# Performance work log

Hardware: AMD Instinct MI355X
Metric: run time of the kernel (lower is better)

Reference implementation:

```python
import jax, jax.numpy as jnp
import numpy as np

N = 100000          # n_nodes
E = 3200000         # n_edges (avg degree 32)
IN_FEATS = 256
H = 128             # h_feats
N_HOPS = 4


def setup_inputs() -> dict:
    key = jax.random.key(0)
    ks = jax.random.split(key, 8)
    edge_index = jax.random.randint(ks[0], (2, E), 0, N, dtype=jnp.int32)
    features = jax.random.normal(ks[1], (N, IN_FEATS), dtype=jnp.float32)
    # input block: Linear(in_feats, h_feats)
    W0 = jax.random.normal(ks[2], (IN_FEATS, H), dtype=jnp.float32) / np.sqrt(IN_FEATS)
    b0 = jnp.zeros((H,), jnp.float32)
    # per-hop GCNConv bias (weight=False because RN=='attentive')
    biases = jnp.zeros((N_HOPS, H), jnp.float32)
    # per-hop attention gate: Linear(2*h_feats, 1) + tanh
    Watt = jax.random.normal(ks[3], (N_HOPS, 2 * H), dtype=jnp.float32) / np.sqrt(2 * H)
    batt = jnp.zeros((N_HOPS,), jnp.float32)
    return {"edge_index": edge_index, "features": features,
            "W0": W0, "b0": b0, "biases": biases, "Watt": Watt, "batt": batt}


def _gcn_agg(x, src, dst):
    # symmetric GCN normalization with self-loops: D^-1/2 (A+I) D^-1/2 @ x
    deg = jnp.zeros((N,), x.dtype).at[dst].add(1.0) + 1.0  # +1 for self-loop
    dinv = jax.lax.rsqrt(deg)
    w = dinv[src] * dinv[dst]                               # [E]
    out = jnp.zeros((N, x.shape[1]), x.dtype).at[dst].add(x[src] * w[:, None])
    return out + x * (dinv * dinv)[:, None]                 # self-loop term


def reference(edge_index, features, W0, b0, biases, Watt, batt):
    src, dst = edge_index[0], edge_index[1]
    # hop-0 input block (dropout=0, norm=Identity)
    h = jax.nn.relu(features @ W0 + b0)                     # [N, H]
    for i in range(N_HOPS):
        # GCNConv with weight=False: aggregation + bias + act
        h_k = jax.nn.relu(_gcn_agg(h, src, dst) + biases[i])
        # attentive hop combination: a = tanh(Linear([h_k, h]))
        a = jnp.tanh(jnp.concatenate([h_k, h], axis=-1) @ Watt[i] + batt[i])[:, None]
        h = a * h_k + (1.0 - a) * h
    return h
```

## Files before the change

### kernel.cpp

```cpp
#include <hip/hip_runtime.h>
#include <hip/hip_fp16.h>
#include <math.h>

#define N_NODES 100000
#define N_EDGES 3200000
#define IN_F 256
#define H 128
#define N_HOPS 4
#define SCAN_B 256
#define GB_M 128
#define GB_K 32


__global__ void deg_kernel(const int* __restrict__ dst, int* __restrict__ deg) {
    int e = blockIdx.x * blockDim.x + threadIdx.x;
    if (e < N_EDGES) atomicAdd(&deg[dst[e]], 1);
}

__global__ void dinv_kernel(const int* __restrict__ deg, float* __restrict__ dinv) {
    int n = blockIdx.x * blockDim.x + threadIdx.x;
    if (n < N_NODES) dinv[n] = rsqrtf((float)deg[n] + 1.0f);
}

__global__ void scan_p1(const int* __restrict__ deg, int* __restrict__ bsum) {
    __shared__ int s[SCAN_B];
    int n = blockIdx.x * SCAN_B + threadIdx.x;
    s[threadIdx.x] = (n < N_NODES) ? deg[n] : 0;
    __syncthreads();
    for (int off = SCAN_B / 2; off; off >>= 1) {
        if (threadIdx.x < off) s[threadIdx.x] += s[threadIdx.x + off];
        __syncthreads();
    }
    if (threadIdx.x == 0) bsum[blockIdx.x] = s[0];
}

__global__ void scan_p2(int* __restrict__ bsum, int nb) {
    __shared__ int s[512];
    int t = threadIdx.x;
    int v0 = (t < nb) ? bsum[t] : 0;
    s[t] = v0;
    __syncthreads();
    for (int off = 1; off < 512; off <<= 1) {
        int v = (t >= off) ? s[t - off] : 0;
        __syncthreads();
        s[t] += v;
        __syncthreads();
    }
    if (t < nb) bsum[t] = s[t] - v0;
}

__global__ void scan_p3(const int* __restrict__ deg, const int* __restrict__ boff,
                        int* __restrict__ rowptr) {
    __shared__ int s[SCAN_B];
    int n = blockIdx.x * SCAN_B + threadIdx.x;
    int v = (n < N_NODES) ? deg[n] : 0;
    s[threadIdx.x] = v;
    __syncthreads();
    for (int off = 1; off < SCAN_B; off <<= 1) {
        int t = (threadIdx.x >= off) ? s[threadIdx.x - off] : 0;
        __syncthreads();
        s[threadIdx.x] += t;
        __syncthreads();
    }
    int incl = s[threadIdx.x];
    int excl = incl - v;
    if (n < N_NODES) rowptr[n] = boff[blockIdx.x] + excl;
    if (n == N_NODES - 1) rowptr[N_NODES] = boff[blockIdx.x] + incl;
}

__global__ void scatter_kernel(const int* __restrict__ src, const int* __restrict__ dst,
                               const float* __restrict__ dinv, const int* __restrict__ rowptr,
                               int* __restrict__ cursor, uint2* __restrict__ edges) {
    int e = blockIdx.x * blockDim.x + threadIdx.x;
    if (e >= N_EDGES) return;
    int s = src[e], d = dst[e];
    int pos = rowptr[d] + atomicAdd(&cursor[d], 1);
    edges[pos] = make_uint2((unsigned)s, __float_as_uint(dinv[s] * dinv[d]));
}

__global__ __launch_bounds__(256) void input_gemm(const float* __restrict__ X,
                                                  const float* __restrict__ W0,
                                                  const float* __restrict__ b0,
                                                  __half* __restrict__ h16) {
    __shared__ float AsT[GB_K][GB_M + 4];
    __shared__ float Ws[GB_K][H];
    int node0 = blockIdx.x * GB_M;
    int tid = threadIdx.x;
    int tx = tid & 15;
    int ty = tid >> 4;

    float acc[8][8];
#pragma unroll
    for (int i = 0; i < 8; ++i)
#pragma unroll
        for (int j = 0; j < 8; ++j) acc[i][j] = 0.f;

    for (int k0 = 0; k0 < IN_F; k0 += GB_K) {
#pragma unroll
        for (int j = 0; j < 4; ++j) {
            int idx = tid + 256 * j;
            int row = idx >> 3, c4 = idx & 7;
            float4 v = make_float4(0.f, 0.f, 0.f, 0.f);
            if (node0 + row < N_NODES)
                v = *(const float4*)(X + (size_t)(node0 + row) * IN_F + k0 + c4 * 4);
            AsT[c4 * 4 + 0][row] = v.x;
            AsT[c4 * 4 + 1][row] = v.y;
            AsT[c4 * 4 + 2][row] = v.z;
            AsT[c4 * 4 + 3][row] = v.w;
        }
#pragma unroll
        for (int j = 0; j < 4; ++j) {
            int idx = tid + 256 * j;
            int row = idx >> 5, c4 = idx & 31;
            *(float4*)&Ws[row][c4 * 4] = *(const float4*)(W0 + (size_t)(k0 + row) * H + c4 * 4);
        }
        __syncthreads();
#pragma unroll
        for (int kk = 0; kk < GB_K; ++kk) {
            float a[8], w[8];
            *(float4*)&a[0] = *(const float4*)&AsT[kk][ty * 8];
            *(float4*)&a[4] = *(const float4*)&AsT[kk][ty * 8 + 4];
            *(float4*)&w[0] = *(const float4*)&Ws[kk][tx * 8];
            *(float4*)&w[4] = *(const float4*)&Ws[kk][tx * 8 + 4];
#pragma unroll
            for (int i = 0; i < 8; ++i)
#pragma unroll
                for (int j = 0; j < 8; ++j) acc[i][j] += a[i] * w[j];
        }
        __syncthreads();
    }

#pragma unroll
    for (int i = 0; i < 8; ++i) {
        int n = node0 + ty * 8 + i;
        if (n < N_NODES) {
            union { float4 f4; __half2 h2[4]; } u;
#pragma unroll
            for (int jj = 0; jj < 4; ++jj) {
                float v0 = acc[i][2 * jj + 0] + b0[tx * 8 + 2 * jj + 0];
                float v1 = acc[i][2 * jj + 1] + b0[tx * 8 + 2 * jj + 1];
                v0 = v0 > 0.f ? v0 : 0.f;
                v1 = v1 > 0.f ? v1 : 0.f;
                u.h2[jj] = __floats2half2_rn(v0, v1);
            }
            *(float4*)(h16 + (size_t)n * H + tx * 8) = u.f4;
        }
    }
}

__global__ __launch_bounds__(256) void hop_kernel(const __half* __restrict__ h_in,
                                                  __half* __restrict__ h16_out,
                                                  float* __restrict__ out32,
                                                  const int* __restrict__ rowptr,
                                                  const uint2* __restrict__ edges,
                                                  const float* __restrict__ dinv,
                                                  const float* __restrict__ bias,
                                                  const float* __restrict__ Wa,
                                                  const float* __restrict__ batt) {
    int wid = threadIdx.x >> 6;
    int lane = threadIdx.x & 63;
    int n = blockIdx.x * 4 + wid;
    if (n >= N_NODES) return;

    float2 hn = __half22float2(((const __half2*)(h_in + (size_t)n * H))[lane]);
    float dd = dinv[n];
    dd = dd * dd;
    float accx = hn.x * dd, accy = hn.y * dd;

    int e0 = rowptr[n], e1 = rowptr[n + 1];
    for (int base = e0; base < e1; base += 64) {
        int cnt = e1 - base;
        if (cnt > 64) cnt = 64;
        int sv = 0;
        float wv = 0.f;
        if (lane < cnt) {
            uint2 ev = edges[base + lane];
            sv = (int)ev.x;
            wv = __uint_as_float(ev.y);
        }
        int j = 0;
        for (; j + 3 < cnt; j += 4) {
            int s0 = __shfl(sv, j + 0), s1 = __shfl(sv, j + 1);
            int s2 = __shfl(sv, j + 2), s3 = __shfl(sv, j + 3);
            float w0 = __shfl(wv, j + 0), w1 = __shfl(wv, j + 1);
            float w2 = __shfl(wv, j + 2), w3 = __shfl(wv, j + 3);
            float2 g0 = __half22float2(((const __half2*)(h_in + (size_t)s0 * H))[lane]);
            float2 g1 = __half22float2(((const __half2*)(h_in + (size_t)s1 * H))[lane]);
            float2 g2 = __half22float2(((const __half2*)(h_in + (size_t)s2 * H))[lane]);
            float2 g3 = __half22float2(((const __half2*)(h_in + (size_t)s3 * H))[lane]);
            accx += w0 * g0.x + w1 * g1.x + w2 * g2.x + w3 * g3.x;
            accy += w0 * g0.y + w1 * g1.y + w2 * g2.y + w3 * g3.y;
        }
        for (; j < cnt; ++j) {
            int sj = __shfl(sv, j);
            float wj = __shfl(wv, j);
            float2 g = __half22float2(((const __half2*)(h_in + (size_t)sj * H))[lane]);
            accx += wj * g.x;
            accy += wj * g.y;
        }
    }

    float hkx = accx + bias[2 * lane];     hkx = hkx > 0.f ? hkx : 0.f;
    float hky = accy + bias[2 * lane + 1]; hky = hky > 0.f ? hky : 0.f;

    float p = hkx * Wa[2 * lane] + hky * Wa[2 * lane + 1]
            + hn.x * Wa[H + 2 * lane] + hn.y * Wa[H + 2 * lane + 1];
#pragma unroll
    for (int off = 32; off; off >>= 1) p += __shfl_xor(p, off);
    float a = tanhf(p + batt[0]);

    float ox = a * hkx + (1.f - a) * hn.x;
    float oy = a * hky + (1.f - a) * hn.y;
    if (out32) {
        ((float2*)(out32 + (size_t)n * H))[lane] = make_float2(ox, oy);
    } else {
        ((__half2*)(h16_out + (size_t)n * H))[lane] = __floats2half2_rn(ox, oy);
    }
}


extern "C" void kernel_launch(void* const* d_in, const int* in_sizes, int n_in,
                              void* d_out, int out_size, void* d_ws, size_t ws_size,
                              hipStream_t stream) {
    const int* edge_index = (const int*)d_in[0];
    const int* src = edge_index;
    const int* dst = edge_index + N_EDGES;
    const float* features = (const float*)d_in[1];
    const float* W0 = (const float*)d_in[2];
    const float* b0 = (const float*)d_in[3];
    const float* biases = (const float*)d_in[4];
    const float* Watt = (const float*)d_in[5];
    const float* batt = (const float*)d_in[6];
    float* out = (float*)d_out;

    size_t off = 0;
    char* base = (char*)d_ws;
    auto carve = [&](size_t bytes) -> void* {
        void* q = base + off;
        off += (bytes + 255) & ~(size_t)255;
        return q;
    };
    int* deg = (int*)carve((size_t)N_NODES * 4);
    float* dinv = (float*)carve((size_t)N_NODES * 4);
    int* rowptr = (int*)carve((size_t)(N_NODES + 1) * 4);
    int* cursor = (int*)carve((size_t)N_NODES * 4);
    int* bsum = (int*)carve(4096);
    uint2* edges = (uint2*)carve((size_t)N_EDGES * 8);
    __half* h16A = (__half*)carve((size_t)N_NODES * H * 2);
    __half* h16B = (__half*)carve((size_t)N_NODES * H * 2);

    hipMemsetAsync(deg, 0, (size_t)N_NODES * 4, stream);
    hipMemsetAsync(cursor, 0, (size_t)N_NODES * 4, stream);

    int eb = (N_EDGES + 255) / 256;
    int nbN = (N_NODES + 255) / 256;
    deg_kernel<<<eb, 256, 0, stream>>>(dst, deg);
    dinv_kernel<<<nbN, 256, 0, stream>>>(deg, dinv);
    scan_p1<<<nbN, SCAN_B, 0, stream>>>(deg, bsum);
    scan_p2<<<1, 512, 0, stream>>>(bsum, nbN);
    scan_p3<<<nbN, SCAN_B, 0, stream>>>(deg, bsum, rowptr);
    scatter_kernel<<<eb, 256, 0, stream>>>(src, dst, dinv, rowptr, cursor, edges);

    input_gemm<<<(N_NODES + GB_M - 1) / GB_M, 256, 0, stream>>>(features, W0, b0, h16A);

    __half* hin = h16A;
    __half* hout = h16B;
    for (int i = 0; i < N_HOPS; ++i) {
        bool last = (i == N_HOPS - 1);
        hop_kernel<<<(N_NODES + 3) / 4, 256, 0, stream>>>(
            hin, hout, last ? out : nullptr, rowptr, edges, dinv,
            biases + (size_t)i * H, Watt + (size_t)i * 2 * H, batt + i);
        __half* t = hin; hin = hout; hout = t;
    }
}
```

Measured before the change: 999.0 us.

## Use two-pass bucketed CSR scatter and MFMA fp16 input GEMM

The single random-scatter CSR build is replaced by two passes. Edges are first binned into buckets of 32 destination nodes, then scattered within each bucket, which improves locality of the atomics and writes. The FP32 SIMT input GEMM is replaced by an MFMA 16x16x32 fp16 GEMM with swizzled LDS tiles, and W0 is converted and transposed to fp16 in a prep kernel. This adds an extra pass over the edges and an fp16 rounding of the inputs. The temporary edge buffer reuses the h16B allocation.

```diff
diff --git a/kernel.cpp b/kernel.cpp
--- a/kernel.cpp
+++ b/kernel.cpp
@@ -8,8 +8,11 @@
 #define H 128
 #define N_HOPS 4
 #define SCAN_B 256
-#define GB_M 128
-#define GB_K 32
+#define BSH 5
+#define NBUCK ((N_NODES + 31) >> BSH)
+
+typedef _Float16 half8_t __attribute__((ext_vector_type(8)));
+typedef float f32x4 __attribute__((ext_vector_type(4)));
 
 
 __global__ void deg_kernel(const int* __restrict__ dst, int* __restrict__ deg) {
@@ -68,84 +71,123 @@
     if (n == N_NODES - 1) rowptr[N_NODES] = boff[blockIdx.x] + incl;
 }
 
-__global__ void scatter_kernel(const int* __restrict__ src, const int* __restrict__ dst,
-                               const float* __restrict__ dinv, const int* __restrict__ rowptr,
-                               int* __restrict__ cursor, uint2* __restrict__ edges) {
+__global__ void bucket_p1(const int* __restrict__ src, const int* __restrict__ dst,
+                          const int* __restrict__ rowptr, int* __restrict__ bcur,
+                          uint2* __restrict__ tmp) {
     int e = blockIdx.x * blockDim.x + threadIdx.x;
     if (e >= N_EDGES) return;
     int s = src[e], d = dst[e];
+    int b = d >> BSH;
+    int pos = rowptr[b << BSH] + atomicAdd(&bcur[b], 1);
+    tmp[pos] = make_uint2((unsigned)s, (unsigned)d);
+}
+
+__global__ void scatter2(const uint2* __restrict__ tmp, const float* __restrict__ dinv,
+                         const int* __restrict__ rowptr, int* __restrict__ cursor,
+                         uint2* __restrict__ edges) {
+    int e = blockIdx.x * blockDim.x + threadIdx.x;
+    if (e >= N_EDGES) return;
+    uint2 ev = tmp[e];
+    int s = (int)ev.x, d = (int)ev.y;
     int pos = rowptr[d] + atomicAdd(&cursor[d], 1);
-    edges[pos] = make_uint2((unsigned)s, __float_as_uint(dinv[s] * dinv[d]));
-}
-
-__global__ __launch_bounds__(256) void input_gemm(const float* __restrict__ X,
-                                                  const float* __restrict__ W0,
-                                                  const float* __restrict__ b0,
-                                                  __half* __restrict__ h16) {
-    __shared__ float AsT[GB_K][GB_M + 4];
-    __shared__ float Ws[GB_K][H];
-    int node0 = blockIdx.x * GB_M;
+    edges[pos] = make_uint2(ev.x, __float_as_uint(dinv[s] * dinv[d]));
+}
+
+__global__ void w16_kernel(const float* __restrict__ W0, _Float16* __restrict__ W16t) {
+    int t = blockIdx.x * 256 + threadIdx.x;
+    if (t < H * IN_F) {
+        int n = t >> 8;
+        int k = t & 255;
+        W16t[(size_t)n * IN_F + k] = (_Float16)W0[(size_t)k * H + n];
+    }
+}
+
+__global__ __launch_bounds__(256) void mfma_gemm(const float* __restrict__ X,
+                                                 const _Float16* __restrict__ W16t,
+                                                 const float* __restrict__ b0,
+                                                 __half* __restrict__ h16) {
+    __shared__ _Float16 Al[128 * 64];
+    __shared__ _Float16 Bl[128 * 64];
     int tid = threadIdx.x;
-    int tx = tid & 15;
-    int ty = tid >> 4;
-
-    float acc[8][8];
-#pragma unroll
-    for (int i = 0; i < 8; ++i)
-#pragma unroll
-        for (int j = 0; j < 8; ++j) acc[i][j] = 0.f;
-
-    for (int k0 = 0; k0 < IN_F; k0 += GB_K) {
+    int wv = tid >> 6, ln = tid & 63;
+    size_t node0 = (size_t)blockIdx.x * 128;
+
+    f32x4 acc[2][8];
+#pragma unroll
+    for (int mi = 0; mi < 2; ++mi)
+#pragma unroll
+        for (int ni = 0; ni < 8; ++ni) acc[mi][ni] = (f32x4)(0.f);
+
+    int arow = tid >> 1;
+    int koff = (tid & 1) * 32;
+    bool arow_ok = (node0 + (size_t)arow) < N_NODES;
+
+    for (int k0 = 0; k0 < IN_F; k0 += 64) {
 #pragma unroll
         for (int j = 0; j < 4; ++j) {
-            int idx = tid + 256 * j;
-            int row = idx >> 3, c4 = idx & 7;
-            float4 v = make_float4(0.f, 0.f, 0.f, 0.f);
-            if (node0 + row < N_NODES)
-                v = *(const float4*)(X + (size_t)(node0 + row) * IN_F + k0 + c4 * 4);
-            AsT[c4 * 4 + 0][row] = v.x;
-            AsT[c4 * 4 + 1][row] = v.y;
-            AsT[c4 * 4 + 2][row] = v.z;
-            AsT[c4 * 4 + 3][row] = v.w;
-        }
-#pragma unroll
-        for (int j = 0; j < 4; ++j) {
-            int idx = tid + 256 * j;
-            int row = idx >> 5, c4 = idx & 31;
-            *(float4*)&Ws[row][c4 * 4] = *(const float4*)(W0 + (size_t)(k0 + row) * H + c4 * 4);
-        }
-        __syncthreads();
-#pragma unroll
-        for (int kk = 0; kk < GB_K; ++kk) {
-            float a[8], w[8];
-            *(float4*)&a[0] = *(const float4*)&AsT[kk][ty * 8];
-            *(float4*)&a[4] = *(const float4*)&AsT[kk][ty * 8 + 4];
-            *(float4*)&w[0] = *(const float4*)&Ws[kk][tx * 8];
-            *(float4*)&w[4] = *(const float4*)&Ws[kk][tx * 8 + 4];
-#pragma unroll
-            for (int i = 0; i < 8; ++i)
-#pragma unroll
-                for (int j = 0; j < 8; ++j) acc[i][j] += a[i] * w[j];
-        }
-        __syncthreads();
-    }
-
-#pragma unroll
-    for (int i = 0; i < 8; ++i) {
-        int n = node0 + ty * 8 + i;
-        if (n < N_NODES) {
-            union { float4 f4; __half2 h2[4]; } u;
-#pragma unroll
-            for (int jj = 0; jj < 4; ++jj) {
-                float v0 = acc[i][2 * jj + 0] + b0[tx * 8 + 2 * jj + 0];
-                float v1 = acc[i][2 * jj + 1] + b0[tx * 8 + 2 * jj + 1];
-                v0 = v0 > 0.f ? v0 : 0.f;
-                v1 = v1 > 0.f ? v1 : 0.f;
-                u.h2[jj] = __floats2half2_rn(v0, v1);
-            }
-            *(float4*)(h16 + (size_t)n * H + tx * 8) = u.f4;
-        }
-    }
+            float4 u0 = make_float4(0.f, 0.f, 0.f, 0.f), u1 = u0;
+            if (arow_ok) {
+                const float4* xp = (const float4*)(X + (node0 + (size_t)arow) * IN_F + k0 + koff + j * 8);
+                u0 = xp[0]; u1 = xp[1];
+            }
+            half8_t hv;
+            hv[0] = (_Float16)u0.x; hv[1] = (_Float16)u0.y;
+            hv[2] = (_Float16)u0.z; hv[3] = (_Float16)u0.w;
+            hv[4] = (_Float16)u1.x; hv[5] = (_Float16)u1.y;
+            hv[6] = (_Float16)u1.z; hv[7] = (_Float16)u1.w;
+            int unit = (koff >> 3) + j;
+            *(half8_t*)&Al[arow * 64 + ((unit ^ (arow & 7)) << 3)] = hv;
+        }
+        {
+            const half8_t* wp = (const half8_t*)(W16t + (size_t)arow * IN_F + k0 + koff);
+#pragma unroll
+            for (int j = 0; j < 4; ++j) {
+                half8_t hv = wp[j];
+                int unit = (koff >> 3) + j;
+                *(half8_t*)&Bl[arow * 64 + ((unit ^ (arow & 7)) << 3)] = hv;
+            }
+        }
+        __syncthreads();
+#pragma unroll
+        for (int ks = 0; ks < 2; ++ks) {
+            int lk = ks * 4 + (ln >> 4);
+            int l15 = ln & 15;
+            half8_t a[2], b[8];
+#pragma unroll
+            for (int mi = 0; mi < 2; ++mi) {
+                int row = wv * 32 + mi * 16 + l15;
+                a[mi] = *(half8_t*)&Al[row * 64 + ((lk ^ (row & 7)) << 3)];
+            }
+#pragma unroll
+            for (int ni = 0; ni < 8; ++ni) {
+                int col = ni * 16 + l15;
+                b[ni] = *(half8_t*)&Bl[col * 64 + ((lk ^ (col & 7)) << 3)];
+            }
+#pragma unroll
+            for (int mi = 0; mi < 2; ++mi)
+#pragma unroll
+                for (int ni = 0; ni < 8; ++ni)
+                    acc[mi][ni] = __builtin_amdgcn_mfma_f32_16x16x32_f16(a[mi], b[ni], acc[mi][ni], 0, 0, 0);
+        }
+        __syncthreads();
+    }
+
+    int cgrp = ln >> 4, ccol = ln & 15;
+#pragma unroll
+    for (int mi = 0; mi < 2; ++mi)
+#pragma unroll
+        for (int ni = 0; ni < 8; ++ni) {
+            int col = ni * 16 + ccol;
+            float bb = b0[col];
+#pragma unroll
+            for (int r = 0; r < 4; ++r) {
+                size_t node = node0 + (size_t)(wv * 32 + mi * 16 + cgrp * 4 + r);
+                if (node < N_NODES) {
+                    float v = acc[mi][ni][r] + bb;
+                    h16[node * H + col] = __float2half(v > 0.f ? v : 0.f);
+                }
+            }
+        }
 }
 
 __global__ __launch_bounds__(256) void hop_kernel(const __half* __restrict__ h_in,
@@ -244,13 +286,17 @@
     float* dinv = (float*)carve((size_t)N_NODES * 4);
     int* rowptr = (int*)carve((size_t)(N_NODES + 1) * 4);
     int* cursor = (int*)carve((size_t)N_NODES * 4);
+    int* bcur = (int*)carve((size_t)NBUCK * 4);
     int* bsum = (int*)carve(4096);
     uint2* edges = (uint2*)carve((size_t)N_EDGES * 8);
+    _Float16* W16t = (_Float16*)carve((size_t)H * IN_F * 2);
     __half* h16A = (__half*)carve((size_t)N_NODES * H * 2);
     __half* h16B = (__half*)carve((size_t)N_NODES * H * 2);
+    uint2* tmp = (uint2*)h16B;
 
     hipMemsetAsync(deg, 0, (size_t)N_NODES * 4, stream);
     hipMemsetAsync(cursor, 0, (size_t)N_NODES * 4, stream);
+    hipMemsetAsync(bcur, 0, (size_t)NBUCK * 4, stream);
 
     int eb = (N_EDGES + 255) / 256;
     int nbN = (N_NODES + 255) / 256;
@@ -259,9 +305,11 @@
     scan_p1<<<nbN, SCAN_B, 0, stream>>>(deg, bsum);
     scan_p2<<<1, 512, 0, stream>>>(bsum, nbN);
     scan_p3<<<nbN, SCAN_B, 0, stream>>>(deg, bsum, rowptr);
-    scatter_kernel<<<eb, 256, 0, stream>>>(src, dst, dinv, rowptr, cursor, edges);
-
-    input_gemm<<<(N_NODES + GB_M - 1) / GB_M, 256, 0, stream>>>(features, W0, b0, h16A);
+    bucket_p1<<<eb, 256, 0, stream>>>(src, dst, rowptr, bcur, tmp);
+    scatter2<<<eb, 256, 0, stream>>>(tmp, dinv, rowptr, cursor, edges);
+
+    w16_kernel<<<(H * IN_F + 255) / 256, 256, 0, stream>>>(W0, W16t);
+    mfma_gemm<<<(N_NODES + 127) / 128, 256, 0, stream>>>(features, W16t, b0, h16A);
 
     __half* hin = h16A;
     __half* hout = h16B;
```

Measured after the change: 1.198 ms. +19.9%, slower.
